# Kernel tuning notes

Hardware: AMD Instinct MI355X
Metric: run time of the kernel (lower is better)

Reference implementation:

```python
import jax, jax.numpy as jnp
import numpy as np

POOL = 8  # kernel_size = [8, 1]: pool factor 8 along H (for *_H) and along W (for *_W)

def _pool_h(x, k):
    B, C, H, W = x.shape
    return x.reshape(B, C, H // k, k, W).mean(axis=3)  # (B,C,H/k,W)

def _pool_w(x, k):
    B, C, H, W = x.shape
    return x.reshape(B, C, H, W // k, k).mean(axis=4)  # (B,C,H,W/k)

def setup_inputs() -> dict:
    key = jax.random.key(0)
    k1, k2 = jax.random.split(key)
    shape = (8, 256, 128, 128)
    return {
        "tensor1": jax.random.normal(k1, shape, dtype=jnp.float32),
        "tensor2": jax.random.normal(k2, shape, dtype=jnp.float32),
    }

def reference(tensor1, tensor2):
    B, C, H, W = tensor1.shape
    kH, kW = H // POOL, W // POOL
    # pooled keys (from tensor1) and values (from tensor2)
    key_H = _pool_h(tensor1, POOL)    # (B,C,kH,W)
    key_W = _pool_w(tensor1, POOL)    # (B,C,H,kW)
    val_H = _pool_h(tensor2, POOL)    # (B,C,kH,W)
    val_W = _pool_w(tensor2, POOL)    # (B,C,H,kW)
    # criss-cross energies: contract over (c, w) for H-branch, (c, h) for W-branch
    energy_H = jnp.einsum('bchw,bckw->bhk', tensor2, key_H).reshape(B, H * kH)
    energy_W = jnp.einsum('bchw,bchk->bwk', tensor2, key_W).reshape(B, W * kW)
    energy = jnp.concatenate([energy_H, energy_W], axis=-1)
    # global (all-element) min-max normalization, then softmax over concat axis
    e_min, e_max = energy.min(), energy.max()
    energy = (energy - e_min) / (e_max - e_min)
    concate = jax.nn.softmax(energy, axis=-1)
    att_H = concate[:, : H * kH].reshape(B, H, kH)
    att_W = concate[:, H * kH :].reshape(B, W, kW)
    out_H = jnp.einsum('bckw,bhk->bchw', val_H, att_H)
    out_W = jnp.einsum('bchk,bwk->bchw', val_W, att_W)
    gamma = jnp.float32(0.5)
    return gamma * (out_H + out_W) + tensor2
```

## Files before the change

### kernel.cpp

```cpp
#include <hip/hip_runtime.h>
#include <cstddef>

#define CC 256
#define HH 128
#define WW 128
#define HW (HH*WW)

typedef __attribute__((ext_vector_type(8))) short short8v;
typedef __attribute__((ext_vector_type(4))) float float4v;

__device__ __forceinline__ short f2bf(float x) {
    unsigned u = __float_as_uint(x);
    u += 0x7FFFu + ((u >> 16) & 1u);
    return (short)(u >> 16);
}
__device__ __forceinline__ float4 add4(float4 a, float4 b) {
    float4 r; r.x=a.x+b.x; r.y=a.y+b.y; r.z=a.z+b.z; r.w=a.w+b.w; return r;
}
__device__ __forceinline__ float4 scale4(float4 a, float s) {
    float4 r; r.x=a.x*s; r.y=a.y*s; r.z=a.z*s; r.w=a.w*s; return r;
}
__device__ __forceinline__ float4 shflx4(float4 v, int m) {
    float4 r;
    r.x = __shfl_xor(v.x, m); r.y = __shfl_xor(v.y, m);
    r.z = __shfl_xor(v.z, m); r.w = __shfl_xor(v.w, m);
    return r;
}
__device__ __forceinline__ float hsum4(float4 v) { return v.x+v.y+v.z+v.w; }

__global__ __launch_bounds__(512, 4) void fused_pool_energy(
    const float* __restrict__ t1, const float* __restrict__ t2,
    unsigned short* __restrict__ valHT, unsigned short* __restrict__ valWbf,
    float* __restrict__ PH, float* __restrict__ PW)
{
    __shared__ __align__(16) short t2lds[64*128];
    __shared__ __align__(16) short t2T  [128*64];
    __shared__ __align__(16) short kH   [16*128];
    __shared__ __align__(16) short kWT  [16*128];

    const int bid = blockIdx.x;
    const int b   = bid & 7;
    const int c   = bid >> 3;
    const int tid = threadIdx.x;
    const int l   = tid & 63;
    const int wv  = tid >> 6;
    const int q   = tid & 31;
    const int g   = tid >> 5;
    const int bc  = b*CC + c;
    const size_t cbase = (size_t)bc * HW;
    const float4* t1c = (const float4*)(t1 + cbase);
    const float4* t2c = (const float4*)(t2 + cbase);

    float4 aR[8];
    #pragma unroll
    for (int r = 0; r < 8; ++r) aR[r] = t1c[g*256 + r*32 + q];
    float4 cR[4];
    #pragma unroll
    for (int r = 0; r < 4; ++r) cR[r] = t2c[g*128 + r*32 + q];

    {
        float4 s = add4(add4(add4(aR[0],aR[1]), add4(aR[2],aR[3])),
                        add4(add4(aR[4],aR[5]), add4(aR[6],aR[7])));
        float4 m4 = scale4(s, 0.125f);
        short4 p; p.x=f2bf(m4.x); p.y=f2bf(m4.y); p.z=f2bf(m4.z); p.w=f2bf(m4.w);
        *(short4*)&kH[g*128 + ((q*4) ^ ((g&7)<<3))] = p;
        const int kw = q >> 1;
        const int sw = (kw & 7) << 3;
        #pragma unroll
        for (int r = 0; r < 8; ++r) {
            float rs = hsum4(aR[r]);
            rs += __shfl_xor(rs, 1);
            if ((l & 1) == 0)
                kWT[kw*128 + ((g*8+r) ^ sw)] = f2bf(rs * 0.125f);
        }
    }
    __syncthreads();

    float4v accH = {0.f,0.f,0.f,0.f};
    float4v accW = {0.f,0.f,0.f,0.f};
    float4 dR[4];

    #pragma unroll
    for (int half = 0; half < 2; ++half) {
        float4 x0, x1, x2, x3;
        if (half == 0) { x0=cR[0]; x1=cR[1]; x2=cR[2]; x3=cR[3]; }
        else           { x0=dR[0]; x1=dR[1]; x2=dR[2]; x3=dR[3]; }

        if (half == 0) {
            #pragma unroll
            for (int r = 0; r < 4; ++r) dR[r] = t2c[2048 + g*128 + r*32 + q];
        }

        {
            float4 sB = add4(add4(x0,x1), add4(x2,x3));
            float4 f8 = add4(sB, shflx4(sB, 32));
            if (l < 32) {
                const int k = half*8 + wv;
                const size_t vb = (size_t)bc * 2048;
                valHT[vb + (q*4+0)*16 + k] = (unsigned short)f2bf(f8.x * 0.125f);
                valHT[vb + (q*4+1)*16 + k] = (unsigned short)f2bf(f8.y * 0.125f);
                valHT[vb + (q*4+2)*16 + k] = (unsigned short)f2bf(f8.z * 0.125f);
                valHT[vb + (q*4+3)*16 + k] = (unsigned short)f2bf(f8.w * 0.125f);
            }
        }
        {
            const int kw = q >> 1;
            float r0 = hsum4(x0), r1 = hsum4(x1), r2 = hsum4(x2), r3 = hsum4(x3);
            r0 += __shfl_xor(r0, 1); r1 += __shfl_xor(r1, 1);
            r2 += __shfl_xor(r2, 1); r3 += __shfl_xor(r3, 1);
            if ((l & 1) == 0) {
                const size_t vb = (size_t)bc*2048 + (size_t)(half*64 + g*4)*16 + kw;
                valWbf[vb +  0] = (unsigned short)f2bf(r0 * 0.125f);
                valWbf[vb + 16] = (unsigned short)f2bf(r1 * 0.125f);
                valWbf[vb + 32] = (unsigned short)f2bf(r2 * 0.125f);
                valWbf[vb + 48] = (unsigned short)f2bf(r3 * 0.125f);
            }
        }
        short4 s0, s1, s2, s3;
        s0.x=f2bf(x0.x); s0.y=f2bf(x0.y); s0.z=f2bf(x0.z); s0.w=f2bf(x0.w);
        s1.x=f2bf(x1.x); s1.y=f2bf(x1.y); s1.z=f2bf(x1.z); s1.w=f2bf(x1.w);
        s2.x=f2bf(x2.x); s2.y=f2bf(x2.y); s2.z=f2bf(x2.z); s2.w=f2bf(x2.w);
        s3.x=f2bf(x3.x); s3.y=f2bf(x3.y); s3.z=f2bf(x3.z); s3.w=f2bf(x3.w);
        {
            const int hl0 = g*4;
            *(short4*)&t2lds[(hl0+0)*128 + ((q*4) ^ (((hl0+0)&7)<<3))] = s0;
            *(short4*)&t2lds[(hl0+1)*128 + ((q*4) ^ (((hl0+1)&7)<<3))] = s1;
            *(short4*)&t2lds[(hl0+2)*128 + ((q*4) ^ (((hl0+2)&7)<<3))] = s2;
            *(short4*)&t2lds[(hl0+3)*128 + ((q*4) ^ (((hl0+3)&7)<<3))] = s3;
            const int swt = (q & 7) << 3;
            const int hb  = hl0 ^ swt;
            short4 p;
            p.x=s0.x; p.y=s1.x; p.z=s2.x; p.w=s3.x;
            *(short4*)&t2T[(q*4+0)*64 + hb] = p;
            p.x=s0.y; p.y=s1.y; p.z=s2.y; p.w=s3.y;
            *(short4*)&t2T[(q*4+1)*64 + hb] = p;
            p.x=s0.z; p.y=s1.z; p.z=s2.z; p.w=s3.z;
            *(short4*)&t2T[(q*4+2)*64 + hb] = p;
            p.x=s0.w; p.y=s1.w; p.z=s2.w; p.w=s3.w;
            *(short4*)&t2T[(q*4+3)*64 + hb] = p;
        }
        __syncthreads();

        if ((wv >> 2) == half) {
            const int hl = (wv & 3)*16 + (l & 15);
            const int kb = l & 15;
            #pragma unroll
            for (int ws2 = 0; ws2 < 4; ++ws2) {
                const int wb = ws2*32 + (l>>4)*8;
                short8v A = *(const short8v*)&t2lds[hl*128 + (wb ^ ((hl&7)<<3))];
                short8v B = *(const short8v*)&kH  [kb*128 + (wb ^ ((kb&7)<<3))];
                accH = __builtin_amdgcn_mfma_f32_16x16x32_bf16(A, B, accH, 0, 0, 0);
            }
        }
        {
            const int kb = l & 15;
            const int w  = wv*16 + (l & 15);
            const int swt = ((w >> 2) & 7) << 3;
            #pragma unroll
            for (int hs = 0; hs < 2; ++hs) {
                const int hloc = hs*32 + (l>>4)*8;
                const int hg   = half*64 + hloc;
                short8v A = *(const short8v*)&kWT[kb*128 + (hg ^ ((kb&7)<<3))];
                short8v B = *(const short8v*)&t2T[w*64   + (hloc ^ swt)];
                accW = __builtin_amdgcn_mfma_f32_16x16x32_bf16(A, B, accW, 0, 0, 0);
            }
        }
        __syncthreads();
    }

    {
        const size_t pb = (size_t)bc * 2048;
        #pragma unroll
        for (int r = 0; r < 4; ++r) {
            const int h = wv*16 + (l>>4)*4 + r;
            PH[pb + h*16 + (l&15)] = accH[r];
            const int k = (l>>4)*4 + r;
            PW[pb + k*128 + wv*16 + (l&15)] = accW[r];
        }
    }
}

__global__ __launch_bounds__(256) void energy_reduce(
    const float* __restrict__ PH, const float* __restrict__ PW,
    float* __restrict__ energy, float* __restrict__ bmin, float* __restrict__ bmax)
{
    const int bidx = blockIdx.x;
    const int tid  = threadIdx.x;
    const int ol   = tid & 63, qd = tid >> 6;
    const int o    = bidx*64 + ol;
    __shared__ float red[4][64];

    const int isW = o >> 14;
    const int oo  = o & 16383;
    const int b   = oo >> 11, i = oo & 2047;
    const float* P = (isW ? PW : PH) + (size_t)b*256*2048 + i;
    float s = 0.f;
    #pragma unroll 8
    for (int j = 0; j < 64; ++j) s += P[(size_t)(qd*64 + j)*2048];
    red[qd][ol] = s;
    __syncthreads();

    if (tid < 64) {
        float v = red[0][tid] + red[1][tid] + red[2][tid] + red[3][tid];
        const int o2 = bidx*64 + tid;
        const int oo2 = o2 & 16383;
        const int b2 = oo2 >> 11, i2 = oo2 & 2047;
        const size_t dst = (o2 >> 14)
            ? ((size_t)b2*4096 + 2048 + (size_t)(i2 & 127)*16 + (i2 >> 7))
            : ((size_t)b2*4096 + i2);
        energy[dst] = v;
        float mn = v, mx = v;
        #pragma unroll
        for (int sft = 32; sft > 0; sft >>= 1) {
            mn = fminf(mn, __shfl_xor(mn, sft));
            mx = fmaxf(mx, __shfl_xor(mx, sft));
        }
        if (tid == 0) { bmin[bidx] = mn; bmax[bidx] = mx; }
    }
}

__global__ __launch_bounds__(1024) void softmax_kernel(
    const float* __restrict__ energy, const float* __restrict__ bmin,
    const float* __restrict__ bmax,
    unsigned short* __restrict__ aHbf, unsigned short* __restrict__ aWbf)
{
    const int b = blockIdx.x, tid = threadIdx.x;
    const int lane = tid & 63, wid = tid >> 6;
    __shared__ float smn[16], smx[16], sred[16], bc2[2];

    float mn = 3.0e38f, mx = -3.0e38f;
    if (tid < 512) { mn = bmin[tid]; mx = bmax[tid]; }
    #pragma unroll
    for (int s = 32; s > 0; s >>= 1) {
        mn = fminf(mn, __shfl_xor(mn, s));
        mx = fmaxf(mx, __shfl_xor(mx, s));
    }
    if (lane == 0) { smn[wid] = mn; smx[wid] = mx; }
    __syncthreads();
    if (tid == 0) {
        float a = smn[0], m = smx[0];
        #pragma unroll
        for (int i = 1; i < 16; ++i) { a = fminf(a, smn[i]); m = fmaxf(m, smx[i]); }
        bc2[0] = a; bc2[1] = m;
    }
    __syncthreads();
    const float gmn = bc2[0];
    const float inv = 1.0f / (bc2[1] - gmn);

    float4 v = ((const float4*)energy)[b*1024 + tid];
    float4 e;
    e.x = __expf((v.x - gmn) * inv);
    e.y = __expf((v.y - gmn) * inv);
    e.z = __expf((v.z - gmn) * inv);
    e.w = __expf((v.w - gmn) * inv);
    float loc = e.x + e.y + e.z + e.w;
    #pragma unroll
    for (int s = 32; s > 0; s >>= 1) loc += __shfl_down(loc, s);
    if (lane == 0) sred[wid] = loc;
    __syncthreads();
    if (tid == 0) {
        float a = 0.f;
        #pragma unroll
        for (int j = 0; j < 16; ++j) a += sred[j];
        bc2[0] = 1.0f / a;
    }
    __syncthreads();
    const float r = bc2[0];
    short4 p;
    p.x = f2bf(e.x * r); p.y = f2bf(e.y * r);
    p.z = f2bf(e.z * r); p.w = f2bf(e.w * r);
    if (tid < 512)
        *(short4*)&aHbf[(size_t)b*2048 + tid*4] = p;
    else
        *(short4*)&aWbf[(size_t)b*2048 + (tid-512)*4] = p;
}

__global__ __launch_bounds__(256) void out_kernel(
    const float* __restrict__ t2,
    const unsigned short* __restrict__ valHT,
    const unsigned short* __restrict__ valWbf,
    const unsigned short* __restrict__ aHbf,
    const unsigned short* __restrict__ aWbf,
    float* __restrict__ out)
{
    const int bid = blockIdx.x;
    const int b = bid & 7, c = bid >> 3;
    const int bc = b*CC + c;
    const int tid = threadIdx.x;
    const int l  = tid & 63;
    const int wv = tid >> 6;
    const int ln = l & 15;
    const int q4 = l >> 4;
    const size_t tb = (size_t)bc * HW;

    const unsigned short* vHT = valHT  + (size_t)bc*2048;
    const unsigned short* vW  = valWbf + (size_t)bc*2048;
    const unsigned short* aH  = aHbf + (size_t)b*2048;
    const unsigned short* aW  = aWbf + (size_t)b*2048;

    short8v Bf[8];
    {
        const unsigned short* src = (q4 < 2) ? vHT : aW;
        #pragma unroll
        for (int tw = 0; tw < 8; ++tw)
            Bf[tw] = *(const short8v*)&src[(tw*16 + ln)*16 + (q4 & 1)*8];
    }

    #pragma unroll
    for (int t = 0; t < 2; ++t) {
        const int th = wv*2 + t;
        const unsigned short* asrc = (q4 < 2) ? aH : vW;
        short8v Af = *(const short8v*)&asrc[(th*16 + ln)*16 + (q4 & 1)*8];
        #pragma unroll
        for (int tw = 0; tw < 8; ++tw) {
            float4v acc = {0.f,0.f,0.f,0.f};
            acc = __builtin_amdgcn_mfma_f32_16x16x32_bf16(Af, Bf[tw], acc, 0, 0, 0);
            const size_t base = tb + (size_t)(th*16 + q4*4)*128 + tw*16 + ln;
            #pragma unroll
            for (int r = 0; r < 4; ++r) {
                const float tv = t2[base + (size_t)r*128];
                out[base + (size_t)r*128] = fmaf(0.5f, acc[r], tv);
            }
        }
    }
}

extern "C" void kernel_launch(void* const* d_in, const int* in_sizes, int n_in,
                              void* d_out, int out_size, void* d_ws, size_t ws_size,
                              hipStream_t stream)
{
    const float* t1 = (const float*)d_in[0];
    const float* t2 = (const float*)d_in[1];
    float* out = (float*)d_out;
    char*  ws  = (char*)d_ws;

    unsigned short* valHT  = (unsigned short*)ws;
    unsigned short* valWbf = (unsigned short*)(ws + ((size_t)8 << 20));
    float* energy = (float*)(ws + ((size_t)16 << 20));
    float* bmin   = energy + 32768;
    float* bmax   = bmin + 512;
    unsigned short* aHbf = (unsigned short*)(ws + ((size_t)17 << 20));
    unsigned short* aWbf = aHbf + 8*2048;

    float* PH = out;
    float* PW = out + (size_t)4194304;

    hipLaunchKernelGGL(fused_pool_energy, dim3(2048), dim3(512), 0, stream,
                       t1, t2, valHT, valWbf, PH, PW);
    hipLaunchKernelGGL(energy_reduce, dim3(512), dim3(256), 0, stream,
                       PH, PW, energy, bmin, bmax);
    hipLaunchKernelGGL(softmax_kernel, dim3(8), dim3(1024), 0, stream,
                       energy, bmin, bmax, aHbf, aWbf);
    hipLaunchKernelGGL(out_kernel, dim3(2048), dim3(256), 0, stream,
                       t2, valHT, valWbf, aHbf, aWbf, out);
}
```

Measured before the change: 140.9 us.

## Halve block size, drop transposed LDS tile, compute W-energy with scalar FMAs

The pool/energy kernel now runs 256-thread blocks instead of 512, and each wave handles both H halves with two MFMA accumulators. The transposed bf16 copy of tensor2 in LDS is removed. The W-branch energy is now computed with per-thread fp32 FMAs against an fp32 pooled-key table, and t1 is streamed instead of held in registers. The goal is lower LDS and register use for higher occupancy, at the cost of much more scalar ALU work and LDS reads in the W-branch.

Result: slower. 161.1 us (+14.3%).

```diff
diff --git a/kernel.cpp b/kernel.cpp
--- a/kernel.cpp
+++ b/kernel.cpp
@@ -14,169 +14,130 @@
     u += 0x7FFFu + ((u >> 16) & 1u);
     return (short)(u >> 16);
 }
+__device__ __forceinline__ float bf2f(unsigned short s) {
+    return __uint_as_float(((unsigned)s) << 16);
+}
 __device__ __forceinline__ float4 add4(float4 a, float4 b) {
     float4 r; r.x=a.x+b.x; r.y=a.y+b.y; r.z=a.z+b.z; r.w=a.w+b.w; return r;
 }
 __device__ __forceinline__ float4 scale4(float4 a, float s) {
     float4 r; r.x=a.x*s; r.y=a.y*s; r.z=a.z*s; r.w=a.w*s; return r;
 }
-__device__ __forceinline__ float4 shflx4(float4 v, int m) {
-    float4 r;
-    r.x = __shfl_xor(v.x, m); r.y = __shfl_xor(v.y, m);
-    r.z = __shfl_xor(v.z, m); r.w = __shfl_xor(v.w, m);
-    return r;
-}
 __device__ __forceinline__ float hsum4(float4 v) { return v.x+v.y+v.z+v.w; }
 
-__global__ __launch_bounds__(512, 4) void fused_pool_energy(
+__global__ __launch_bounds__(256, 5) void fused_pool_energy(
     const float* __restrict__ t1, const float* __restrict__ t2,
     unsigned short* __restrict__ valHT, unsigned short* __restrict__ valWbf,
     float* __restrict__ PH, float* __restrict__ PW)
 {
     __shared__ __align__(16) short t2lds[64*128];
-    __shared__ __align__(16) short t2T  [128*64];
-    __shared__ __align__(16) short kH   [16*128];
-    __shared__ __align__(16) short kWT  [16*128];
+    __shared__ __align__(16) short kH  [16*128];
+    __shared__ __align__(16) float kWf [128*16];
 
     const int bid = blockIdx.x;
-    const int b   = bid & 7;
-    const int c   = bid >> 3;
+    const int b = bid & 7, c = bid >> 3;
+    const int bc = b*CC + c;
     const int tid = threadIdx.x;
     const int l   = tid & 63;
     const int wv  = tid >> 6;
     const int q   = tid & 31;
     const int g   = tid >> 5;
-    const int bc  = b*CC + c;
-    const size_t cbase = (size_t)bc * HW;
-    const float4* t1c = (const float4*)(t1 + cbase);
-    const float4* t2c = (const float4*)(t2 + cbase);
-
-    float4 aR[8];
-    #pragma unroll
-    for (int r = 0; r < 8; ++r) aR[r] = t1c[g*256 + r*32 + q];
-    float4 cR[4];
-    #pragma unroll
-    for (int r = 0; r < 4; ++r) cR[r] = t2c[g*128 + r*32 + q];
-
-    {
-        float4 s = add4(add4(add4(aR[0],aR[1]), add4(aR[2],aR[3])),
-                        add4(add4(aR[4],aR[5]), add4(aR[6],aR[7])));
+    const float4* t1c = (const float4*)(t1 + (size_t)bc * HW);
+    const float4* t2c = (const float4*)(t2 + (size_t)bc * HW);
+
+    #pragma unroll
+    for (int tt = 0; tt < 2; ++tt) {
+        const int k = g + tt*8;
+        const float4* p = t1c + k*256 + q;
+        float4 s = {0.f,0.f,0.f,0.f};
+        #pragma unroll
+        for (int j = 0; j < 8; ++j) s = add4(s, p[j*32]);
         float4 m4 = scale4(s, 0.125f);
-        short4 p; p.x=f2bf(m4.x); p.y=f2bf(m4.y); p.z=f2bf(m4.z); p.w=f2bf(m4.w);
-        *(short4*)&kH[g*128 + ((q*4) ^ ((g&7)<<3))] = p;
-        const int kw = q >> 1;
-        const int sw = (kw & 7) << 3;
-        #pragma unroll
-        for (int r = 0; r < 8; ++r) {
-            float rs = hsum4(aR[r]);
+        short4 pk; pk.x=f2bf(m4.x); pk.y=f2bf(m4.y); pk.z=f2bf(m4.z); pk.w=f2bf(m4.w);
+        *(short4*)&kH[k*128 + ((q*4) ^ ((k&7)<<3))] = pk;
+    }
+    #pragma unroll
+    for (int j = 0; j < 8; ++j) {
+        const int t = tid + j*256;
+        const int h = t >> 4, kx = t & 15;
+        const float4* p = t1c + h*32 + kx*2;
+        kWf[h*16 + kx] = (hsum4(p[0]) + hsum4(p[1])) * 0.125f;
+    }
+    __syncthreads();
+
+    float4v accHa = {0.f,0.f,0.f,0.f};
+    float4v accHb = {0.f,0.f,0.f,0.f};
+    float accW[8];
+    #pragma unroll
+    for (int i = 0; i < 8; ++i) accW[i] = 0.f;
+    const int wcol = tid & 127;
+    const int kg   = tid >> 7;
+
+    #pragma unroll
+    for (int half = 0; half < 2; ++half) {
+        float4 colsum = {0.f,0.f,0.f,0.f};
+        #pragma unroll
+        for (int j = 0; j < 8; ++j) {
+            const int hl = g*8 + j;
+            float4 x = t2c[(half*64 + hl)*32 + q];
+            colsum = add4(colsum, x);
+            short4 pk; pk.x=f2bf(x.x); pk.y=f2bf(x.y); pk.z=f2bf(x.z); pk.w=f2bf(x.w);
+            *(short4*)&t2lds[hl*128 + ((q*4) ^ ((hl&7)<<3))] = pk;
+            float rs = hsum4(x);
             rs += __shfl_xor(rs, 1);
             if ((l & 1) == 0)
-                kWT[kw*128 + ((g*8+r) ^ sw)] = f2bf(rs * 0.125f);
-        }
-    }
-    __syncthreads();
-
-    float4v accH = {0.f,0.f,0.f,0.f};
-    float4v accW = {0.f,0.f,0.f,0.f};
-    float4 dR[4];
-
-    #pragma unroll
-    for (int half = 0; half < 2; ++half) {
-        float4 x0, x1, x2, x3;
-        if (half == 0) { x0=cR[0]; x1=cR[1]; x2=cR[2]; x3=cR[3]; }
-        else           { x0=dR[0]; x1=dR[1]; x2=dR[2]; x3=dR[3]; }
-
-        if (half == 0) {
+                valWbf[(size_t)bc*2048 + (size_t)(half*64 + hl)*16 + (q>>1)] =
+                    (unsigned short)f2bf(rs * 0.125f);
+        }
+        {
+            float4 m4 = scale4(colsum, 0.125f);
+            const int k = half*8 + g;
+            const size_t vb = (size_t)bc * 2048;
+            valHT[vb + (q*4+0)*16 + k] = (unsigned short)f2bf(m4.x);
+            valHT[vb + (q*4+1)*16 + k] = (unsigned short)f2bf(m4.y);
+            valHT[vb + (q*4+2)*16 + k] = (unsigned short)f2bf(m4.z);
+            valHT[vb + (q*4+3)*16 + k] = (unsigned short)f2bf(m4.w);
+        }
+        __syncthreads();
+
+        {
+            const int hl = wv*16 + (l & 15);
+            const int kb = l & 15;
+            float4v& accH = half ? accHb : accHa;
             #pragma unroll
-            for (int r = 0; r < 4; ++r) dR[r] = t2c[2048 + g*128 + r*32 + q];
-        }
-
-        {
-            float4 sB = add4(add4(x0,x1), add4(x2,x3));
-            float4 f8 = add4(sB, shflx4(sB, 32));
-            if (l < 32) {
-                const int k = half*8 + wv;
-                const size_t vb = (size_t)bc * 2048;
-                valHT[vb + (q*4+0)*16 + k] = (unsigned short)f2bf(f8.x * 0.125f);
-                valHT[vb + (q*4+1)*16 + k] = (unsigned short)f2bf(f8.y * 0.125f);
-                valHT[vb + (q*4+2)*16 + k] = (unsigned short)f2bf(f8.z * 0.125f);
-                valHT[vb + (q*4+3)*16 + k] = (unsigned short)f2bf(f8.w * 0.125f);
-            }
-        }
-        {
-            const int kw = q >> 1;
-            float r0 = hsum4(x0), r1 = hsum4(x1), r2 = hsum4(x2), r3 = hsum4(x3);
-            r0 += __shfl_xor(r0, 1); r1 += __shfl_xor(r1, 1);
-            r2 += __shfl_xor(r2, 1); r3 += __shfl_xor(r3, 1);
-            if ((l & 1) == 0) {
-                const size_t vb = (size_t)bc*2048 + (size_t)(half*64 + g*4)*16 + kw;
-                valWbf[vb +  0] = (unsigned short)f2bf(r0 * 0.125f);
-                valWbf[vb + 16] = (unsigned short)f2bf(r1 * 0.125f);
-                valWbf[vb + 32] = (unsigned short)f2bf(r2 * 0.125f);
-                valWbf[vb + 48] = (unsigned short)f2bf(r3 * 0.125f);
-            }
-        }
-        short4 s0, s1, s2, s3;
-        s0.x=f2bf(x0.x); s0.y=f2bf(x0.y); s0.z=f2bf(x0.z); s0.w=f2bf(x0.w);
-        s1.x=f2bf(x1.x); s1.y=f2bf(x1.y); s1.z=f2bf(x1.z); s1.w=f2bf(x1.w);
-        s2.x=f2bf(x2.x); s2.y=f2bf(x2.y); s2.z=f2bf(x2.z); s2.w=f2bf(x2.w);
-        s3.x=f2bf(x3.x); s3.y=f2bf(x3.y); s3.z=f2bf(x3.z); s3.w=f2bf(x3.w);
-        {
-            const int hl0 = g*4;
-            *(short4*)&t2lds[(hl0+0)*128 + ((q*4) ^ (((hl0+0)&7)<<3))] = s0;
-            *(short4*)&t2lds[(hl0+1)*128 + ((q*4) ^ (((hl0+1)&7)<<3))] = s1;
-            *(short4*)&t2lds[(hl0+2)*128 + ((q*4) ^ (((hl0+2)&7)<<3))] = s2;
-            *(short4*)&t2lds[(hl0+3)*128 + ((q*4) ^ (((hl0+3)&7)<<3))] = s3;
-            const int swt = (q & 7) << 3;
-            const int hb  = hl0 ^ swt;
-            short4 p;
-            p.x=s0.x; p.y=s1.x; p.z=s2.x; p.w=s3.x;
-            *(short4*)&t2T[(q*4+0)*64 + hb] = p;
-            p.x=s0.y; p.y=s1.y; p.z=s2.y; p.w=s3.y;
-            *(short4*)&t2T[(q*4+1)*64 + hb] = p;
-            p.x=s0.z; p.y=s1.z; p.z=s2.z; p.w=s3.z;
-            *(short4*)&t2T[(q*4+2)*64 + hb] = p;
-            p.x=s0.w; p.y=s1.w; p.z=s2.w; p.w=s3.w;
-            *(short4*)&t2T[(q*4+3)*64 + hb] = p;
-        }
-        __syncthreads();
-
-        if ((wv >> 2) == half) {
-            const int hl = (wv & 3)*16 + (l & 15);
-            const int kb = l & 15;
-            #pragma unroll
-            for (int ws2 = 0; ws2 < 4; ++ws2) {
-                const int wb = ws2*32 + (l>>4)*8;
+            for (int ch = 0; ch < 4; ++ch) {
+                const int wb = ch*32 + (l>>4)*8;
                 short8v A = *(const short8v*)&t2lds[hl*128 + (wb ^ ((hl&7)<<3))];
                 short8v B = *(const short8v*)&kH  [kb*128 + (wb ^ ((kb&7)<<3))];
                 accH = __builtin_amdgcn_mfma_f32_16x16x32_bf16(A, B, accH, 0, 0, 0);
             }
         }
         {
-            const int kb = l & 15;
-            const int w  = wv*16 + (l & 15);
-            const int swt = ((w >> 2) & 7) << 3;
-            #pragma unroll
-            for (int hs = 0; hs < 2; ++hs) {
-                const int hloc = hs*32 + (l>>4)*8;
-                const int hg   = half*64 + hloc;
-                short8v A = *(const short8v*)&kWT[kb*128 + (hg ^ ((kb&7)<<3))];
-                short8v B = *(const short8v*)&t2T[w*64   + (hloc ^ swt)];
-                accW = __builtin_amdgcn_mfma_f32_16x16x32_bf16(A, B, accW, 0, 0, 0);
+            #pragma unroll 8
+            for (int row = 0; row < 64; ++row) {
+                float x = bf2f((unsigned short)
+                    t2lds[row*128 + (wcol ^ ((row&7)<<3))]);
+                const float* kr = &kWf[(half*64 + row)*16 + kg*8];
+                #pragma unroll
+                for (int d = 0; d < 8; ++d)
+                    accW[d] = fmaf(x, kr[d], accW[d]);
             }
         }
         __syncthreads();
     }
 
+    const size_t pb = (size_t)bc * 2048;
     {
-        const size_t pb = (size_t)bc * 2048;
+        const int hb = wv*16 + (l>>4)*4;
+        const int kc = l & 15;
         #pragma unroll
         for (int r = 0; r < 4; ++r) {
-            const int h = wv*16 + (l>>4)*4 + r;
-            PH[pb + h*16 + (l&15)] = accH[r];
-            const int k = (l>>4)*4 + r;
-            PW[pb + k*128 + wv*16 + (l&15)] = accW[r];
-        }
+            PH[pb + (size_t)(hb + r)*16 + kc]      = accHa[r];
+            PH[pb + (size_t)(64 + hb + r)*16 + kc] = accHb[r];
+        }
+        #pragma unroll
+        for (int d = 0; d < 8; ++d)
+            PW[pb + (size_t)(kg*8 + d)*128 + wcol] = accW[d];
     }
 }
 
@@ -345,7 +306,7 @@
     float* PH = out;
     float* PW = out + (size_t)4194304;
 
-    hipLaunchKernelGGL(fused_pool_energy, dim3(2048), dim3(512), 0, stream,
+    hipLaunchKernelGGL(fused_pool_energy, dim3(2048), dim3(256), 0, stream,
                        t1, t2, valHT, valWbf, PH, PW);
     hipLaunchKernelGGL(energy_reduce, dim3(512), dim3(256), 0, stream,
                        PH, PW, energy, bmin, bmax);
```

## Process two channels per block to halve energy partials and reduction work

Applied to the files above, without the earlier changes.

The fused pooling/energy kernel now loops over two channels per block, accumulating MFMA energy partials in registers across both, so the grid halves to 1024 blocks. The number of per-channel partial energy rows written and later summed drops by half, and energy_reduce sums 32 rows per thread instead of 64. It also restructures the global loads to stream t1 and t2 in row chunks per half instead of preloading, drops the occupancy hint, and changes the t2T swizzle. The cost is less parallelism and longer serial work per block, with more syncthreads.

New measurement: 130.8 us. 1.08x faster.

```diff
diff --git a/kernel.cpp b/kernel.cpp
--- a/kernel.cpp
+++ b/kernel.cpp
@@ -28,7 +28,7 @@
 }
 __device__ __forceinline__ float hsum4(float4 v) { return v.x+v.y+v.z+v.w; }
 
-__global__ __launch_bounds__(512, 4) void fused_pool_energy(
+__global__ __launch_bounds__(512) void fused_pool_energy(
     const float* __restrict__ t1, const float* __restrict__ t2,
     unsigned short* __restrict__ valHT, unsigned short* __restrict__ valWbf,
     float* __restrict__ PH, float* __restrict__ PW)
@@ -38,144 +38,147 @@
     __shared__ __align__(16) short kH   [16*128];
     __shared__ __align__(16) short kWT  [16*128];
 
-    const int bid = blockIdx.x;
-    const int b   = bid & 7;
-    const int c   = bid >> 3;
-    const int tid = threadIdx.x;
-    const int l   = tid & 63;
-    const int wv  = tid >> 6;
-    const int q   = tid & 31;
-    const int g   = tid >> 5;
-    const int bc  = b*CC + c;
-    const size_t cbase = (size_t)bc * HW;
-    const float4* t1c = (const float4*)(t1 + cbase);
-    const float4* t2c = (const float4*)(t2 + cbase);
-
-    float4 aR[8];
-    #pragma unroll
-    for (int r = 0; r < 8; ++r) aR[r] = t1c[g*256 + r*32 + q];
-    float4 cR[4];
-    #pragma unroll
-    for (int r = 0; r < 4; ++r) cR[r] = t2c[g*128 + r*32 + q];
-
-    {
-        float4 s = add4(add4(add4(aR[0],aR[1]), add4(aR[2],aR[3])),
-                        add4(add4(aR[4],aR[5]), add4(aR[6],aR[7])));
-        float4 m4 = scale4(s, 0.125f);
-        short4 p; p.x=f2bf(m4.x); p.y=f2bf(m4.y); p.z=f2bf(m4.z); p.w=f2bf(m4.w);
-        *(short4*)&kH[g*128 + ((q*4) ^ ((g&7)<<3))] = p;
-        const int kw = q >> 1;
-        const int sw = (kw & 7) << 3;
-        #pragma unroll
-        for (int r = 0; r < 8; ++r) {
-            float rs = hsum4(aR[r]);
-            rs += __shfl_xor(rs, 1);
-            if ((l & 1) == 0)
-                kWT[kw*128 + ((g*8+r) ^ sw)] = f2bf(rs * 0.125f);
-        }
-    }
-    __syncthreads();
+    const int bid   = blockIdx.x;
+    const int b     = bid & 7;
+    const int chunk = bid >> 3;
+    const int c0    = chunk * 2;
+    const int tid   = threadIdx.x;
+    const int l     = tid & 63;
+    const int v     = tid >> 6;
+    const int w4    = l & 31;
+    const int rq    = l >> 5;
 
     float4v accH = {0.f,0.f,0.f,0.f};
     float4v accW = {0.f,0.f,0.f,0.f};
-    float4 dR[4];
-
-    #pragma unroll
-    for (int half = 0; half < 2; ++half) {
-        float4 x0, x1, x2, x3;
-        if (half == 0) { x0=cR[0]; x1=cR[1]; x2=cR[2]; x3=cR[3]; }
-        else           { x0=dR[0]; x1=dR[1]; x2=dR[2]; x3=dR[3]; }
-
-        if (half == 0) {
-            #pragma unroll
-            for (int r = 0; r < 4; ++r) dR[r] = t2c[2048 + g*128 + r*32 + q];
-        }
-
-        {
-            float4 sB = add4(add4(x0,x1), add4(x2,x3));
-            float4 f8 = add4(sB, shflx4(sB, 32));
-            if (l < 32) {
-                const int k = half*8 + wv;
+
+    for (int ci = 0; ci < 2; ++ci) {
+        const int c = c0 + ci;
+        const int bc = b*CC + c;
+        const size_t cbase = (size_t)bc * HW;
+
+        #pragma unroll
+        for (int half = 0; half < 2; ++half) {
+            const int hbase = half*64 + v*8 + rq*4;
+            const float4* src = (const float4*)(t1 + cbase + (size_t)hbase * WW) + w4;
+            float4 x0 = src[0], x1 = src[32], x2 = src[64], x3 = src[96];
+            float4 s4 = add4(add4(x0,x1), add4(x2,x3));
+            float4 m4 = scale4(add4(s4, shflx4(s4,32)), 0.125f);
+            if (rq == 0) {
+                const int k = half*8 + v;
+                short4 p; p.x=f2bf(m4.x); p.y=f2bf(m4.y); p.z=f2bf(m4.z); p.w=f2bf(m4.w);
+                *(short4*)&kH[k*128 + ((w4*4) ^ ((k&7)<<3))] = p;
+            }
+            float rs0 = hsum4(x0), rs1 = hsum4(x1), rs2 = hsum4(x2), rs3 = hsum4(x3);
+            float o0 = __shfl_xor(rs0,1), o1 = __shfl_xor(rs1,1);
+            float o2 = __shfl_xor(rs2,1), o3 = __shfl_xor(rs3,1);
+            if ((l & 1) == 0) {
+                const int kw = w4 >> 1;
+                const int sw = (kw & 7) << 3;
+                kWT[kw*128 + ((hbase+0) ^ sw)] = f2bf((rs0+o0)*0.125f);
+                kWT[kw*128 + ((hbase+1) ^ sw)] = f2bf((rs1+o1)*0.125f);
+                kWT[kw*128 + ((hbase+2) ^ sw)] = f2bf((rs2+o2)*0.125f);
+                kWT[kw*128 + ((hbase+3) ^ sw)] = f2bf((rs3+o3)*0.125f);
+            }
+        }
+        __syncthreads();
+
+        #pragma unroll
+        for (int half = 0; half < 2; ++half) {
+            const int hbase = half*64 + v*8 + rq*4;
+            const int hl4   = v*8 + rq*4;
+            const float4* src = (const float4*)(t2 + cbase + (size_t)hbase * WW) + w4;
+            float4 x0 = src[0], x1 = src[32], x2 = src[64], x3 = src[96];
+
+            float4 s4 = add4(add4(x0,x1), add4(x2,x3));
+            float4 m4 = scale4(add4(s4, shflx4(s4,32)), 0.125f);
+            if (rq == 0) {
+                const int k = half*8 + v;
                 const size_t vb = (size_t)bc * 2048;
-                valHT[vb + (q*4+0)*16 + k] = (unsigned short)f2bf(f8.x * 0.125f);
-                valHT[vb + (q*4+1)*16 + k] = (unsigned short)f2bf(f8.y * 0.125f);
-                valHT[vb + (q*4+2)*16 + k] = (unsigned short)f2bf(f8.z * 0.125f);
-                valHT[vb + (q*4+3)*16 + k] = (unsigned short)f2bf(f8.w * 0.125f);
-            }
-        }
-        {
-            const int kw = q >> 1;
-            float r0 = hsum4(x0), r1 = hsum4(x1), r2 = hsum4(x2), r3 = hsum4(x3);
-            r0 += __shfl_xor(r0, 1); r1 += __shfl_xor(r1, 1);
-            r2 += __shfl_xor(r2, 1); r3 += __shfl_xor(r3, 1);
-            if ((l & 1) == 0) {
-                const size_t vb = (size_t)bc*2048 + (size_t)(half*64 + g*4)*16 + kw;
-                valWbf[vb +  0] = (unsigned short)f2bf(r0 * 0.125f);
-                valWbf[vb + 16] = (unsigned short)f2bf(r1 * 0.125f);
-                valWbf[vb + 32] = (unsigned short)f2bf(r2 * 0.125f);
-                valWbf[vb + 48] = (unsigned short)f2bf(r3 * 0.125f);
-            }
-        }
-        short4 s0, s1, s2, s3;
-        s0.x=f2bf(x0.x); s0.y=f2bf(x0.y); s0.z=f2bf(x0.z); s0.w=f2bf(x0.w);
-        s1.x=f2bf(x1.x); s1.y=f2bf(x1.y); s1.z=f2bf(x1.z); s1.w=f2bf(x1.w);
-        s2.x=f2bf(x2.x); s2.y=f2bf(x2.y); s2.z=f2bf(x2.z); s2.w=f2bf(x2.w);
-        s3.x=f2bf(x3.x); s3.y=f2bf(x3.y); s3.z=f2bf(x3.z); s3.w=f2bf(x3.w);
-        {
-            const int hl0 = g*4;
-            *(short4*)&t2lds[(hl0+0)*128 + ((q*4) ^ (((hl0+0)&7)<<3))] = s0;
-            *(short4*)&t2lds[(hl0+1)*128 + ((q*4) ^ (((hl0+1)&7)<<3))] = s1;
-            *(short4*)&t2lds[(hl0+2)*128 + ((q*4) ^ (((hl0+2)&7)<<3))] = s2;
-            *(short4*)&t2lds[(hl0+3)*128 + ((q*4) ^ (((hl0+3)&7)<<3))] = s3;
-            const int swt = (q & 7) << 3;
-            const int hb  = hl0 ^ swt;
-            short4 p;
-            p.x=s0.x; p.y=s1.x; p.z=s2.x; p.w=s3.x;
-            *(short4*)&t2T[(q*4+0)*64 + hb] = p;
-            p.x=s0.y; p.y=s1.y; p.z=s2.y; p.w=s3.y;
-            *(short4*)&t2T[(q*4+1)*64 + hb] = p;
-            p.x=s0.z; p.y=s1.z; p.z=s2.z; p.w=s3.z;
-            *(short4*)&t2T[(q*4+2)*64 + hb] = p;
-            p.x=s0.w; p.y=s1.w; p.z=s2.w; p.w=s3.w;
-            *(short4*)&t2T[(q*4+3)*64 + hb] = p;
-        }
-        __syncthreads();
-
-        if ((wv >> 2) == half) {
-            const int hl = (wv & 3)*16 + (l & 15);
-            const int kb = l & 15;
-            #pragma unroll
-            for (int ws2 = 0; ws2 < 4; ++ws2) {
-                const int wb = ws2*32 + (l>>4)*8;
-                short8v A = *(const short8v*)&t2lds[hl*128 + (wb ^ ((hl&7)<<3))];
-                short8v B = *(const short8v*)&kH  [kb*128 + (wb ^ ((kb&7)<<3))];
-                accH = __builtin_amdgcn_mfma_f32_16x16x32_bf16(A, B, accH, 0, 0, 0);
-            }
-        }
-        {
-            const int kb = l & 15;
-            const int w  = wv*16 + (l & 15);
-            const int swt = ((w >> 2) & 7) << 3;
-            #pragma unroll
-            for (int hs = 0; hs < 2; ++hs) {
-                const int hloc = hs*32 + (l>>4)*8;
-                const int hg   = half*64 + hloc;
-                short8v A = *(const short8v*)&kWT[kb*128 + (hg ^ ((kb&7)<<3))];
-                short8v B = *(const short8v*)&t2T[w*64   + (hloc ^ swt)];
-                accW = __builtin_amdgcn_mfma_f32_16x16x32_bf16(A, B, accW, 0, 0, 0);
-            }
-        }
-        __syncthreads();
+                valHT[vb + (w4*4+0)*16 + k] = (unsigned short)f2bf(m4.x);
+                valHT[vb + (w4*4+1)*16 + k] = (unsigned short)f2bf(m4.y);
+                valHT[vb + (w4*4+2)*16 + k] = (unsigned short)f2bf(m4.z);
+                valHT[vb + (w4*4+3)*16 + k] = (unsigned short)f2bf(m4.w);
+            }
+            {
+                float rs0 = hsum4(x0), rs1 = hsum4(x1), rs2 = hsum4(x2), rs3 = hsum4(x3);
+                float o0 = __shfl_xor(rs0,1), o1 = __shfl_xor(rs1,1);
+                float o2 = __shfl_xor(rs2,1), o3 = __shfl_xor(rs3,1);
+                if ((l & 1) == 0) {
+                    const int kw = w4 >> 1;
+                    const size_t vb = (size_t)bc*2048 + (size_t)hbase*16 + kw;
+                    valWbf[vb +  0] = (unsigned short)f2bf((rs0+o0)*0.125f);
+                    valWbf[vb + 16] = (unsigned short)f2bf((rs1+o1)*0.125f);
+                    valWbf[vb + 32] = (unsigned short)f2bf((rs2+o2)*0.125f);
+                    valWbf[vb + 48] = (unsigned short)f2bf((rs3+o3)*0.125f);
+                }
+            }
+            short s0x=f2bf(x0.x), s0y=f2bf(x0.y), s0z=f2bf(x0.z), s0w=f2bf(x0.w);
+            short s1x=f2bf(x1.x), s1y=f2bf(x1.y), s1z=f2bf(x1.z), s1w=f2bf(x1.w);
+            short s2x=f2bf(x2.x), s2y=f2bf(x2.y), s2z=f2bf(x2.z), s2w=f2bf(x2.w);
+            short s3x=f2bf(x3.x), s3y=f2bf(x3.y), s3z=f2bf(x3.z), s3w=f2bf(x3.w);
+            {
+                short4 p;
+                p.x=s0x; p.y=s0y; p.z=s0z; p.w=s0w;
+                *(short4*)&t2lds[(hl4+0)*128 + ((w4*4) ^ (((hl4+0)&7)<<3))] = p;
+                p.x=s1x; p.y=s1y; p.z=s1z; p.w=s1w;
+                *(short4*)&t2lds[(hl4+1)*128 + ((w4*4) ^ (((hl4+1)&7)<<3))] = p;
+                p.x=s2x; p.y=s2y; p.z=s2z; p.w=s2w;
+                *(short4*)&t2lds[(hl4+2)*128 + ((w4*4) ^ (((hl4+2)&7)<<3))] = p;
+                p.x=s3x; p.y=s3y; p.z=s3z; p.w=s3w;
+                *(short4*)&t2lds[(hl4+3)*128 + ((w4*4) ^ (((hl4+3)&7)<<3))] = p;
+            }
+            {
+                short4 p;
+                int w = w4*4 + 0;
+                p.x=s0x; p.y=s1x; p.z=s2x; p.w=s3x;
+                *(short4*)&t2T[w*64 + (hl4 ^ (((w>>1)&7)<<3))] = p;
+                w = w4*4 + 1;
+                p.x=s0y; p.y=s1y; p.z=s2y; p.w=s3y;
+                *(short4*)&t2T[w*64 + (hl4 ^ (((w>>1)&7)<<3))] = p;
+                w = w4*4 + 2;
+                p.x=s0z; p.y=s1z; p.z=s2z; p.w=s3z;
+                *(short4*)&t2T[w*64 + (hl4 ^ (((w>>1)&7)<<3))] = p;
+                w = w4*4 + 3;
+                p.x=s0w; p.y=s1w; p.z=s2w; p.w=s3w;
+                *(short4*)&t2T[w*64 + (hl4 ^ (((w>>1)&7)<<3))] = p;
+            }
+            __syncthreads();
+
+            if ((v >> 2) == half) {
+                const int hl = (v & 3)*16 + (l & 15);
+                const int kb = l & 15;
+                #pragma unroll
+                for (int ws2 = 0; ws2 < 4; ++ws2) {
+                    const int wb = ws2*32 + (l>>4)*8;
+                    short8v A  = *(const short8v*)&t2lds[hl*128 + (wb ^ ((hl&7)<<3))];
+                    short8v B  = *(const short8v*)&kH  [kb*128 + (wb ^ ((kb&7)<<3))];
+                    accH = __builtin_amdgcn_mfma_f32_16x16x32_bf16(A, B, accH, 0, 0, 0);
+                }
+            }
+            {
+                const int kb = l & 15;
+                const int w  = v*16 + (l & 15);
+                #pragma unroll
+                for (int hs = 0; hs < 2; ++hs) {
+                    const int hloc = hs*32 + (l>>4)*8;
+                    const int hg   = half*64 + hloc;
+                    short8v A = *(const short8v*)&kWT[kb*128 + (hg  ^ ((kb&7)<<3))];
+                    short8v B = *(const short8v*)&t2T[w*64   + (hloc ^ (((w>>1)&7)<<3))];
+                    accW = __builtin_amdgcn_mfma_f32_16x16x32_bf16(A, B, accW, 0, 0, 0);
+                }
+            }
+            __syncthreads();
+        }
     }
 
     {
-        const size_t pb = (size_t)bc * 2048;
+        const size_t pb = ((size_t)(b*128 + chunk)) * 2048;
         #pragma unroll
         for (int r = 0; r < 4; ++r) {
-            const int h = wv*16 + (l>>4)*4 + r;
+            const int h = v*16 + (l>>4)*4 + r;
             PH[pb + h*16 + (l&15)] = accH[r];
             const int k = (l>>4)*4 + r;
-            PW[pb + k*128 + wv*16 + (l&15)] = accW[r];
+            PW[pb + k*128 + v*16 + (l&15)] = accW[r];
         }
     }
 }
@@ -193,10 +196,10 @@
     const int isW = o >> 14;
     const int oo  = o & 16383;
     const int b   = oo >> 11, i = oo & 2047;
-    const float* P = (isW ? PW : PH) + (size_t)b*256*2048 + i;
+    const float* P = (isW ? PW : PH) + (size_t)b*128*2048 + i;
     float s = 0.f;
-    #pragma unroll 8
-    for (int j = 0; j < 64; ++j) s += P[(size_t)(qd*64 + j)*2048];
+    #pragma unroll
+    for (int j = 0; j < 32; ++j) s += P[(size_t)(qd*32 + j)*2048];
     red[qd][ol] = s;
     __syncthreads();
 
@@ -343,9 +346,9 @@
     unsigned short* aWbf = aHbf + 8*2048;
 
     float* PH = out;
-    float* PW = out + (size_t)4194304;
-
-    hipLaunchKernelGGL(fused_pool_energy, dim3(2048), dim3(512), 0, stream,
+    float* PW = out + (size_t)2097152;
+
+    hipLaunchKernelGGL(fused_pool_energy, dim3(1024), dim3(512), 0, stream,
                        t1, t2, valHT, valWbf, PH, PW);
     hipLaunchKernelGGL(energy_reduce, dim3(512), dim3(256), 0, stream,
                        PH, PW, energy, bmin, bmax);
```
